# Kernel tuning notes

Hardware: AMD Instinct MI355X
Metric: run time of the kernel (lower is better)

Reference implementation:

```python
import jax, jax.numpy as jnp
import numpy as np

NUM_CLASSES = 19
EPS_MEAN = 1e-6   # torch: denominator eps in per-class mean
EPS_COS = 1e-8    # torch CosineSimilarity default eps


def _nearest_resize_labels(target, H, W):
    # torch nn.Upsample(mode='nearest'): in_idx = floor(out_idx * in / out)
    th, tw = target.shape[1], target.shape[2]
    ih = (jnp.arange(H) * th) // H
    iw = (jnp.arange(W) * tw) // W
    return target[:, ih][:, :, iw]  # [B,H,W]


def _class_centers(feat, lab):
    # feat: [B,C,H,W]; lab: [B,H,W] int. Single-pass segment mean by class,
    # then scatter means back to pixels whose label is in [0, NUM_CLASSES).
    B, C, H, W = feat.shape
    f = feat.reshape(B, C, H * W)                 # [B,C,N]
    l = lab.reshape(B, H * W)                      # [B,N]
    onehot = jax.nn.one_hot(l, NUM_CLASSES, dtype=feat.dtype)  # [B,N,K]; out-of-range -> all-zero row
    sums = jnp.einsum('bcn,bnk->bck', f, onehot)   # per-class channel sums
    counts = onehot.sum(axis=1)                    # [B,K]
    means = sums / (counts[:, None, :] + EPS_MEAN) # [B,C,K]
    gathered = jnp.einsum('bck,bnk->bcn', means, onehot)  # mean at each valid pixel, 0 elsewhere
    valid = (l >= 0) & (l < NUM_CLASSES)           # [B,N]
    center = jnp.where(valid[:, None, :], gathered, f)
    return center.reshape(B, C, H, W)


def _cosine_dim1(a, b):
    # torch CosineSimilarity(dim=1): dot / (max(||a||,eps) * max(||b||,eps))
    num = (a * b).sum(axis=1)
    na = jnp.sqrt((a * a).sum(axis=1))
    nb = jnp.sqrt((b * b).sum(axis=1))
    return num / (jnp.maximum(na, EPS_COS) * jnp.maximum(nb, EPS_COS))


def setup_inputs() -> dict:
    key = jax.random.key(0)
    k1, k2, k3 = jax.random.split(key, 3)
    B, C, H, W = 8, 512, 64, 64
    preds_S = jax.random.normal(k1, (B, C, H, W), dtype=jnp.float32)
    preds_T = jax.random.normal(k2, (B, C, H, W), dtype=jnp.float32)
    target = jax.random.randint(k3, (B, 512, 512), 0, NUM_CLASSES, dtype=jnp.int64)
    return {"preds_S": preds_S, "preds_T": preds_T, "target": target}


def reference(preds_S, preds_T, target):
    H, W = preds_S.shape[2], preds_S.shape[3]
    lab = _nearest_resize_labels(target, H, W)     # [B,H,W]
    center_S = _class_centers(preds_S, lab)
    center_T = _class_centers(preds_T, lab)
    pcsim_S = _cosine_dim1(preds_S, center_S)      # [B,H,W]
    pcsim_T = _cosine_dim1(preds_T, center_T)
    return jnp.mean((pcsim_S - pcsim_T) ** 2)
```

## Files before the change

kernel.cpp:

```cpp
#include <hip/hip_runtime.h>

#define NCLS   19
#define NB     8
#define NC     512
#define NHW    4096
#define EPSM   1e-6f
#define EPSC   1e-8f
#define LBLK   8

#define OFF_LABELS   0u
#define OFF_COUNTS   131072u
#define OFF_SUMS_S   132096u
#define OFF_SUMS_T   443392u
#define OFF_NORM_S   754688u
#define OFF_NORM_T   755712u
#define OFF_PART     756736u

template<int CTRL>
__device__ __forceinline__ float dpp_add(float x) {
    int y = __builtin_amdgcn_update_dpp(0, __float_as_int(x), CTRL, 0xf, 0xf, false);
    return x + __int_as_float(y);
}
__device__ __forceinline__ float wave64_sum(float x) {
    x = dpp_add<0x111>(x);
    x = dpp_add<0x112>(x);
    x = dpp_add<0x114>(x);
    x = dpp_add<0x118>(x);
    x = dpp_add<0x142>(x);
    x = dpp_add<0x143>(x);
    return x;
}

__global__ __launch_bounds__(256) void k_labels(const int* __restrict__ target,
                                                int* __restrict__ labels,
                                                float* __restrict__ counts) {
    __shared__ int hist[NCLS];
    const int blk = blockIdx.x;
    const int b    = blk >> 3;
    const int part = blk & (LBLK - 1);
    const int t = threadIdx.x;
    if (t < NCLS) hist[t] = 0;
    __syncthreads();
    const int* tb = target + (size_t)b * 512 * 512;
    #pragma unroll
    for (int i = 0; i < 2; ++i) {
        int n = part * 512 + t + i * 256;
        int y = n >> 6, x = n & 63;
        int l = tb[(y * 8) * 512 + x * 8];
        labels[b * NHW + n] = l;
        if (l >= 0 && l < NCLS) atomicAdd(&hist[l], 1);
    }
    __syncthreads();
    if (t < NCLS && hist[t] > 0)
        atomicAdd(&counts[b * NCLS + t], (float)hist[t]);
}

__global__ __launch_bounds__(256) void k_sums(const float* __restrict__ fS,
                                              const float* __restrict__ fT,
                                              const int* __restrict__ labels,
                                              float* __restrict__ sumsS,
                                              float* __restrict__ sumsT) {
    __shared__ float2 acc[NCLS * 256];
    const int t   = threadIdx.x;
    const int blk = blockIdx.x;
    const int b   = blk >> 9;
    const int c   = blk & (NC - 1);

    const int4*   lab4 = (const int4*)(labels + b * NHW);
    const float4* pS   = (const float4*)(fS + ((size_t)(b * NC) + c) * NHW);
    const float4* pT   = (const float4*)(fT + ((size_t)(b * NC) + c) * NHW);

    int4 lab[4]; float4 vS[4]; float4 vT[4];
    #pragma unroll
    for (int j = 0; j < 4; ++j) {
        lab[j] = lab4[t + (j << 8)];
        vS[j]  = pS[t + (j << 8)];
        vT[j]  = pT[t + (j << 8)];
    }
    __builtin_amdgcn_sched_barrier(0);

    {
        float4* av = (float4*)acc;
        const float4 z = make_float4(0.f, 0.f, 0.f, 0.f);
        for (int i = t; i < NCLS * 128; i += 256) av[i] = z;
    }
    __syncthreads();

    float2* a0 = acc + t;

    #pragma unroll
    for (int j = 0; j < 4; ++j) {
        const int4   l = lab[j];
        const float4 s = vS[j];
        const float4 u = vT[j];
        if ((unsigned)l.x < NCLS) { float2 v = a0[l.x << 8]; v.x += s.x; v.y += u.x; a0[l.x << 8] = v; }
        if ((unsigned)l.y < NCLS) { float2 v = a0[l.y << 8]; v.x += s.y; v.y += u.y; a0[l.y << 8] = v; }
        if ((unsigned)l.z < NCLS) { float2 v = a0[l.z << 8]; v.x += s.z; v.y += u.z; a0[l.z << 8] = v; }
        if ((unsigned)l.w < NCLS) { float2 v = a0[l.w << 8]; v.x += s.w; v.y += u.w; a0[l.w << 8] = v; }
    }
    __syncthreads();

    const int w = t >> 6, lane = t & 63;
    for (int r = w; r < NCLS; r += 4) {
        const float2* row = acc + r * 256;
        const float2 p0 = row[lane], p1 = row[lane + 64];
        const float2 p2 = row[lane + 128], p3 = row[lane + 192];
        float sx = (p0.x + p1.x) + (p2.x + p3.x);
        float sy = (p0.y + p1.y) + (p2.y + p3.y);
        sx = wave64_sum(sx);
        sy = wave64_sum(sy);
        if (lane == 63) {
            sumsS[((size_t)(b * NCLS + r)) * NC + c] = sx;
            sumsT[((size_t)(b * NCLS + r)) * NC + c] = sy;
        }
    }
}

__global__ __launch_bounds__(64) void k_means(float* __restrict__ sumsS,
                                              float* __restrict__ sumsT,
                                              const float* __restrict__ counts,
                                              float* __restrict__ normS,
                                              float* __restrict__ normT) {
    const int bk = blockIdx.x;
    const int t = threadIdx.x;
    const float inv = 1.f / (counts[bk] + EPSM);
    float* rS = sumsS + (size_t)bk * NC;
    float* rT = sumsT + (size_t)bk * NC;
    float aS = 0.f, aT = 0.f;
    #pragma unroll
    for (int i = 0; i < NC / 64; ++i) {
        float mS = rS[t + i * 64] * inv; rS[t + i * 64] = mS; aS += mS * mS;
        float mT = rT[t + i * 64] * inv; rT[t + i * 64] = mT; aT += mT * mT;
    }
    aS = wave64_sum(aS);
    aT = wave64_sum(aT);
    if (t == 63) { normS[bk] = sqrtf(aS); normT[bk] = sqrtf(aT); }
}

#define CCH 64
__global__ __launch_bounds__(256) void k_dots(const float* __restrict__ fS,
                                              const float* __restrict__ fT,
                                              const float* __restrict__ meansS,
                                              const float* __restrict__ meansT,
                                              const int* __restrict__ labels,
                                              float* __restrict__ part) {
    __shared__ float mS[NCLS * 65];
    __shared__ float mT[NCLS * 65];
    const int blk = blockIdx.x;
    const int chunk = blk & 7;
    const int tile  = (blk >> 3) & 15;
    const int b     = blk >> 7;
    const int t = threadIdx.x;
    const int c0 = chunk * CCH;
    const int n = tile * 256 + t;

    for (int i = t; i < NCLS * CCH; i += 256) {
        const int k = i >> 6, j = i & 63;
        mS[k * 65 + j] = meansS[((size_t)(b * NCLS + k)) * NC + c0 + j];
        mT[k * 65 + j] = meansT[((size_t)(b * NCLS + k)) * NC + c0 + j];
    }
    __syncthreads();

    const int l = labels[b * NHW + n];
    const int lc = (l >= 0 && l < NCLS) ? l : 0;
    const float* pS = fS + ((size_t)(b * NC + c0)) * NHW + n;
    const float* pT = fT + ((size_t)(b * NC + c0)) * NHW + n;
    float dS = 0.f, nS = 0.f, dT = 0.f, nT = 0.f;
    #pragma unroll 8
    for (int ci = 0; ci < CCH; ++ci) {
        const float vS = pS[(size_t)ci * NHW];
        const float vT = pT[(size_t)ci * NHW];
        const float ms = mS[lc * 65 + ci];
        const float mt = mT[lc * 65 + ci];
        dS += vS * ms; nS += vS * vS;
        dT += vT * mt; nT += vT * vT;
    }
    const int p = b * NHW + n;
    part[((size_t)(0 * 8 + chunk)) * (NB * NHW) + p] = dS;
    part[((size_t)(1 * 8 + chunk)) * (NB * NHW) + p] = nS;
    part[((size_t)(2 * 8 + chunk)) * (NB * NHW) + p] = dT;
    part[((size_t)(3 * 8 + chunk)) * (NB * NHW) + p] = nT;
}

__global__ __launch_bounds__(256) void k_final(const float* __restrict__ part,
                                               const int* __restrict__ labels,
                                               const float* __restrict__ normS,
                                               const float* __restrict__ normT,
                                               float* __restrict__ out) {
    __shared__ float red[4];
    const int p = blockIdx.x * 256 + threadIdx.x;
    const int b = p >> 12;
    float dS = 0.f, nS = 0.f, dT = 0.f, nT = 0.f;
    #pragma unroll
    for (int ch = 0; ch < 8; ++ch) {
        dS += part[((size_t)(0 * 8 + ch)) * (NB * NHW) + p];
        nS += part[((size_t)(1 * 8 + ch)) * (NB * NHW) + p];
        dT += part[((size_t)(2 * 8 + ch)) * (NB * NHW) + p];
        nT += part[((size_t)(3 * 8 + ch)) * (NB * NHW) + p];
    }
    const int l = labels[p];
    float val = 0.f;
    if (l >= 0 && l < NCLS) {
        float cS = dS / (fmaxf(sqrtf(nS), EPSC) * fmaxf(normS[b * NCLS + l], EPSC));
        float cT = dT / (fmaxf(sqrtf(nT), EPSC) * fmaxf(normT[b * NCLS + l], EPSC));
        float d = cS - cT;
        val = d * d;
    }
    val = wave64_sum(val);
    if ((threadIdx.x & 63) == 63) red[threadIdx.x >> 6] = val;
    __syncthreads();
    if (threadIdx.x == 0)
        atomicAdd(out, (red[0] + red[1] + red[2] + red[3]) * (1.f / (NB * NHW)));
}

extern "C" void kernel_launch(void* const* d_in, const int* in_sizes, int n_in,
                              void* d_out, int out_size, void* d_ws, size_t ws_size,
                              hipStream_t stream) {
    (void)in_sizes; (void)n_in; (void)out_size; (void)ws_size;
    const float* fS     = (const float*)d_in[0];
    const float* fT     = (const float*)d_in[1];
    const int*   target = (const int*)d_in[2];

    char* ws = (char*)d_ws;
    int*   labels = (int*)  (ws + OFF_LABELS);
    float* counts = (float*)(ws + OFF_COUNTS);
    float* sumsS  = (float*)(ws + OFF_SUMS_S);
    float* sumsT  = (float*)(ws + OFF_SUMS_T);
    float* normS  = (float*)(ws + OFF_NORM_S);
    float* normT  = (float*)(ws + OFF_NORM_T);
    float* part   = (float*)(ws + OFF_PART);

    hipMemsetAsync(d_out, 0, sizeof(float), stream);
    hipMemsetAsync(counts, 0, NB * NCLS * sizeof(float), stream);

    k_labels<<<NB * LBLK, 256, 0, stream>>>(target, labels, counts);
    k_sums  <<<NB * NC, 256, 0, stream>>>(fS, fT, labels, sumsS, sumsT);
    k_means <<<NB * NCLS, 64, 0, stream>>>(sumsS, sumsT, counts, normS, normT);
    k_dots  <<<NB * 16 * 8, 256, 0, stream>>>(fS, fT, sumsS, sumsT, labels, part);
    k_final <<<NB * NHW / 256, 256, 0, stream>>>(part, labels, normS, normT,
                                                 (float*)d_out);
}
```

Baseline: 189.1 us.

## Fuse final cosine reduction into dots kernel and drop memsets

Merges k_final into k_dots: each block now covers 64 pixels across all 512 channels, with four waves splitting the channels and reducing their partials in shared memory, so the partial-sum buffer round trip through global memory goes away. k_labels uses one block per batch and writes counts directly, which removes the counts memset. The output zeroing moves into k_means, which removes the other memset. This cuts two memsets and one kernel launch but gives fewer, longer blocks in k_labels (8) and k_dots (512), which may lower memory-level parallelism.

```diff
diff --git a/kernel.cpp b/kernel.cpp
--- a/kernel.cpp
+++ b/kernel.cpp
@@ -6,7 +6,6 @@
 #define NHW    4096
 #define EPSM   1e-6f
 #define EPSC   1e-8f
-#define LBLK   8
 
 #define OFF_LABELS   0u
 #define OFF_COUNTS   131072u
@@ -14,7 +13,6 @@
 #define OFF_SUMS_T   443392u
 #define OFF_NORM_S   754688u
 #define OFF_NORM_T   755712u
-#define OFF_PART     756736u
 
 template<int CTRL>
 __device__ __forceinline__ float dpp_add(float x) {
@@ -35,24 +33,21 @@
                                                 int* __restrict__ labels,
                                                 float* __restrict__ counts) {
     __shared__ int hist[NCLS];
-    const int blk = blockIdx.x;
-    const int b    = blk >> 3;
-    const int part = blk & (LBLK - 1);
+    const int b = blockIdx.x;
     const int t = threadIdx.x;
     if (t < NCLS) hist[t] = 0;
     __syncthreads();
     const int* tb = target + (size_t)b * 512 * 512;
     #pragma unroll
-    for (int i = 0; i < 2; ++i) {
-        int n = part * 512 + t + i * 256;
+    for (int i = 0; i < 16; ++i) {
+        int n = t + i * 256;
         int y = n >> 6, x = n & 63;
         int l = tb[(y * 8) * 512 + x * 8];
         labels[b * NHW + n] = l;
         if (l >= 0 && l < NCLS) atomicAdd(&hist[l], 1);
     }
     __syncthreads();
-    if (t < NCLS && hist[t] > 0)
-        atomicAdd(&counts[b * NCLS + t], (float)hist[t]);
+    if (t < NCLS) counts[b * NCLS + t] = (float)hist[t];
 }
 
 __global__ __launch_bounds__(256) void k_sums(const float* __restrict__ fS,
@@ -120,9 +115,11 @@
                                               float* __restrict__ sumsT,
                                               const float* __restrict__ counts,
                                               float* __restrict__ normS,
-                                              float* __restrict__ normT) {
+                                              float* __restrict__ normT,
+                                              float* __restrict__ out) {
     const int bk = blockIdx.x;
     const int t = threadIdx.x;
+    if (bk == 0 && t == 0) *out = 0.f;
     const float inv = 1.f / (counts[bk] + EPSM);
     float* rS = sumsS + (size_t)bk * NC;
     float* rT = sumsT + (size_t)bk * NC;
@@ -137,80 +134,73 @@
     if (t == 63) { normS[bk] = sqrtf(aS); normT[bk] = sqrtf(aT); }
 }
 
-#define CCH 64
 __global__ __launch_bounds__(256) void k_dots(const float* __restrict__ fS,
                                               const float* __restrict__ fT,
                                               const float* __restrict__ meansS,
                                               const float* __restrict__ meansT,
                                               const int* __restrict__ labels,
-                                              float* __restrict__ part) {
-    __shared__ float mS[NCLS * 65];
-    __shared__ float mT[NCLS * 65];
-    const int blk = blockIdx.x;
-    const int chunk = blk & 7;
-    const int tile  = (blk >> 3) & 15;
-    const int b     = blk >> 7;
-    const int t = threadIdx.x;
-    const int c0 = chunk * CCH;
-    const int n = tile * 256 + t;
-
-    for (int i = t; i < NCLS * CCH; i += 256) {
-        const int k = i >> 6, j = i & 63;
-        mS[k * 65 + j] = meansS[((size_t)(b * NCLS + k)) * NC + c0 + j];
-        mT[k * 65 + j] = meansT[((size_t)(b * NCLS + k)) * NC + c0 + j];
-    }
-    __syncthreads();
-
-    const int l = labels[b * NHW + n];
+                                              const float* __restrict__ normS,
+                                              const float* __restrict__ normT,
+                                              float* __restrict__ out) {
+    __shared__ float2 mST[4 * NCLS * 65];
+    __shared__ float4 red[4 * 64];
+    const int t    = threadIdx.x;
+    const int w    = t >> 6, px = t & 63;
+    const int blk  = blockIdx.x;
+    const int b    = blk >> 6;
+    const int tile = blk & 63;
+    const int n    = tile * 64 + px;
+
+    const int l  = labels[b * NHW + n];
     const int lc = (l >= 0 && l < NCLS) ? l : 0;
-    const float* pS = fS + ((size_t)(b * NC + c0)) * NHW + n;
-    const float* pT = fT + ((size_t)(b * NC + c0)) * NHW + n;
+
     float dS = 0.f, nS = 0.f, dT = 0.f, nT = 0.f;
-    #pragma unroll 8
-    for (int ci = 0; ci < CCH; ++ci) {
-        const float vS = pS[(size_t)ci * NHW];
-        const float vT = pT[(size_t)ci * NHW];
-        const float ms = mS[lc * 65 + ci];
-        const float mt = mT[lc * 65 + ci];
-        dS += vS * ms; nS += vS * vS;
-        dT += vT * mt; nT += vT * vT;
-    }
-    const int p = b * NHW + n;
-    part[((size_t)(0 * 8 + chunk)) * (NB * NHW) + p] = dS;
-    part[((size_t)(1 * 8 + chunk)) * (NB * NHW) + p] = nS;
-    part[((size_t)(2 * 8 + chunk)) * (NB * NHW) + p] = dT;
-    part[((size_t)(3 * 8 + chunk)) * (NB * NHW) + p] = nT;
-}
-
-__global__ __launch_bounds__(256) void k_final(const float* __restrict__ part,
-                                               const int* __restrict__ labels,
-                                               const float* __restrict__ normS,
-                                               const float* __restrict__ normT,
-                                               float* __restrict__ out) {
-    __shared__ float red[4];
-    const int p = blockIdx.x * 256 + threadIdx.x;
-    const int b = p >> 12;
-    float dS = 0.f, nS = 0.f, dT = 0.f, nT = 0.f;
-    #pragma unroll
-    for (int ch = 0; ch < 8; ++ch) {
-        dS += part[((size_t)(0 * 8 + ch)) * (NB * NHW) + p];
-        nS += part[((size_t)(1 * 8 + ch)) * (NB * NHW) + p];
-        dT += part[((size_t)(2 * 8 + ch)) * (NB * NHW) + p];
-        nT += part[((size_t)(3 * 8 + ch)) * (NB * NHW) + p];
-    }
-    const int l = labels[p];
-    float val = 0.f;
-    if (l >= 0 && l < NCLS) {
-        float cS = dS / (fmaxf(sqrtf(nS), EPSC) * fmaxf(normS[b * NCLS + l], EPSC));
-        float cT = dT / (fmaxf(sqrtf(nT), EPSC) * fmaxf(normT[b * NCLS + l], EPSC));
-        float d = cS - cT;
-        val = d * d;
-    }
-    val = wave64_sum(val);
-    if ((threadIdx.x & 63) == 63) red[threadIdx.x >> 6] = val;
-    __syncthreads();
-    if (threadIdx.x == 0)
-        atomicAdd(out, (red[0] + red[1] + red[2] + red[3]) * (1.f / (NB * NHW)));
+    #pragma unroll
+    for (int r = 0; r < 2; ++r) {
+        __syncthreads();
+        for (int i = t; i < 4 * NCLS * 64; i += 256) {
+            const int ww  = i / (NCLS * 64);
+            const int rem = i - ww * (NCLS * 64);
+            const int k   = rem >> 6, ci = rem & 63;
+            const int c   = ww * 128 + r * 64 + ci;
+            mST[(ww * NCLS + k) * 65 + ci] = make_float2(
+                meansS[((size_t)(b * NCLS + k)) * NC + c],
+                meansT[((size_t)(b * NCLS + k)) * NC + c]);
+        }
+        __syncthreads();
+        const size_t base = ((size_t)(b * NC) + w * 128 + r * 64) * NHW + tile * 64 + px;
+        const float* pS = fS + base;
+        const float* pT = fT + base;
+        const float2* m0 = mST + (w * NCLS + lc) * 65;
+        #pragma unroll 8
+        for (int ci = 0; ci < 64; ++ci) {
+            const float vS = pS[(size_t)ci * NHW];
+            const float vT = pT[(size_t)ci * NHW];
+            const float2 m = m0[ci];
+            dS += vS * m.x; nS += vS * vS;
+            dT += vT * m.y; nT += vT * vT;
+        }
+    }
+    red[w * 64 + px] = make_float4(dS, nS, dT, nT);
+    __syncthreads();
+
+    if (w == 0) {
+        const float4 a0 = red[px],       a1 = red[64 + px];
+        const float4 a2 = red[128 + px], a3 = red[192 + px];
+        const float DS = (a0.x + a1.x) + (a2.x + a3.x);
+        const float NS = (a0.y + a1.y) + (a2.y + a3.y);
+        const float DT = (a0.z + a1.z) + (a2.z + a3.z);
+        const float NT = (a0.w + a1.w) + (a2.w + a3.w);
+        float val = 0.f;
+        if (l >= 0 && l < NCLS) {
+            const float cS = DS / (fmaxf(sqrtf(NS), EPSC) * fmaxf(normS[b * NCLS + l], EPSC));
+            const float cT = DT / (fmaxf(sqrtf(NT), EPSC) * fmaxf(normT[b * NCLS + l], EPSC));
+            const float d = cS - cT;
+            val = d * d;
+        }
+        val = wave64_sum(val);
+        if (px == 63) atomicAdd(out, val * (1.f / (NB * NHW)));
+    }
 }
 
 extern "C" void kernel_launch(void* const* d_in, const int* in_sizes, int n_in,
@@ -228,15 +218,11 @@
     float* sumsT  = (float*)(ws + OFF_SUMS_T);
     float* normS  = (float*)(ws + OFF_NORM_S);
     float* normT  = (float*)(ws + OFF_NORM_T);
-    float* part   = (float*)(ws + OFF_PART);
-
-    hipMemsetAsync(d_out, 0, sizeof(float), stream);
-    hipMemsetAsync(counts, 0, NB * NCLS * sizeof(float), stream);
-
-    k_labels<<<NB * LBLK, 256, 0, stream>>>(target, labels, counts);
+
+    k_labels<<<NB, 256, 0, stream>>>(target, labels, counts);
     k_sums  <<<NB * NC, 256, 0, stream>>>(fS, fT, labels, sumsS, sumsT);
-    k_means <<<NB * NCLS, 64, 0, stream>>>(sumsS, sumsT, counts, normS, normT);
-    k_dots  <<<NB * 16 * 8, 256, 0, stream>>>(fS, fT, sumsS, sumsT, labels, part);
-    k_final <<<NB * NHW / 256, 256, 0, stream>>>(part, labels, normS, normT,
-                                                 (float*)d_out);
-}
+    k_means <<<NB * NCLS, 64, 0, stream>>>(sumsS, sumsT, counts, normS, normT,
+                                           (float*)d_out);
+    k_dots  <<<NB * 64, 256, 0, stream>>>(fS, fT, sumsS, sumsT, labels,
+                                          normS, normT, (float*)d_out);
+}
```

After: 194.8 us. +3.0%, slower.
